# Performance work log

Measured on AMD Instinct MI355X. Metric: run time of the kernel, lower is better.

## Reference

```python
import jax, jax.numpy as jnp
import numpy as np

MARGIN = 0.3
HARD_FACTOR = 0.0
EPS = 1e-6


def setup_inputs() -> dict:
    key = jax.random.key(0)
    k1, k2 = jax.random.split(key)
    inputs = jax.random.normal(k1, (4096, 256), dtype=jnp.float32)
    targets = jax.random.randint(k2, (4096,), 0, 512, dtype=jnp.int64)
    return {"inputs": inputs, "targets": targets}


def reference(inputs, targets):
    n = inputs.shape[0]
    half = n // 2
    # L2-normalize features (matches normalize(): x / (||x|| + 1e-6))
    x = inputs / (jnp.linalg.norm(inputs, axis=-1, keepdims=True) + EPS)
    # pairwise euclidean distances, clamped at 1e-6 before sqrt
    sq = jnp.sum(x * x, axis=1)                      # (n,)
    dist = sq[:, None] + sq[None, :] - 2.0 * (x @ x.T)  # (n, n)
    dist = jnp.sqrt(jnp.clip(dist, EPS))
    # same-identity mask
    mask = targets[:, None] == targets[None, :]      # (n, n) bool
    # rows in the first half mine over columns [half:n], rows in the
    # second half mine over columns [0:half] -> gather the opposite half
    first = (jnp.arange(n) < half)[:, None]          # (n, 1)
    d_o = jnp.where(first, dist[:, half:], dist[:, :half])  # (n, half)
    m_o = jnp.where(first, mask[:, half:], mask[:, :half])  # (n, half) bool
    pos_any = jnp.any(m_o, axis=1)
    neg_any = jnp.any(~m_o, axis=1)
    dist_ap = jnp.where(pos_any,
                        jnp.max(jnp.where(m_o, d_o, -jnp.inf), axis=1),
                        0.0)
    dist_an = jnp.where(neg_any,
                        jnp.min(jnp.where(m_o, jnp.inf, d_o), axis=1),
                        1.0)
    dist_ap = dist_ap * (1.0 + HARD_FACTOR)
    dist_an = dist_an * (1.0 - HARD_FACTOR)
    # MarginRankingLoss(margin)(dist_an, dist_ap, y=1) =
    #   mean(relu(-(dist_an - dist_ap) + margin))
    loss = jnp.mean(jax.nn.relu(dist_ap - dist_an + MARGIN))
    return loss
```

## Files before the change

### kernel.cpp

```cpp
#include <hip/hip_runtime.h>
#include <math.h>

#define N 4096
#define D 256
#define HALF 2048
#define MARGIN 0.3f

#define BM 64
#define NTJ 32

typedef __attribute__((ext_vector_type(8))) short bf16x8;
typedef __attribute__((ext_vector_type(4))) float f32x4;

typedef __attribute__((address_space(1))) const unsigned int gas_uint;
typedef __attribute__((address_space(3))) unsigned int las_uint;

__device__ __forceinline__ void gld16(const unsigned short* g, unsigned short* l) {
    __builtin_amdgcn_global_load_lds((gas_uint*)g, (las_uint*)l, 16, 0, 0);
}

__device__ __forceinline__ unsigned short f2bf(float x) {
    unsigned int u = __float_as_uint(x);
    return (unsigned short)((u + 0x7fffu + ((u >> 16) & 1u)) >> 16);
}

__global__ __launch_bounds__(256) void k_norm(const float* __restrict__ in,
                                              unsigned short* __restrict__ xnb,
                                              float* __restrict__ sq,
                                              unsigned int* __restrict__ cnt) {
    const int row = blockIdx.x * 4 + (threadIdx.x >> 6);
    const int lane = threadIdx.x & 63;
    const float4 v = *(const float4*)&in[(size_t)row * D + lane * 4];
    float s = v.x * v.x + v.y * v.y + v.z * v.z + v.w * v.w;
#pragma unroll
    for (int o = 1; o < 64; o <<= 1) s += __shfl_xor(s, o, 64);
    float nrm = sqrtf(s);
    float inv = 1.0f / (nrm + 1e-6f);
    ushort4 o4;
    o4.x = f2bf(v.x * inv);
    o4.y = f2bf(v.y * inv);
    o4.z = f2bf(v.z * inv);
    o4.w = f2bf(v.w * inv);
    *(ushort4*)&xnb[(size_t)row * D + lane * 4] = o4;
    if (lane == 0) {
        float q = nrm * inv;
        sq[row] = q * q;
    }
    if (blockIdx.x == 0 && threadIdx.x == 0) *cnt = 0u;
}

__global__ __launch_bounds__(256, 2) void k_tile(const unsigned short* __restrict__ xnb,
                                                 const float* __restrict__ sq,
                                                 const int* __restrict__ tg,
                                                 int* __restrict__ rp_ap,
                                                 int* __restrict__ rp_an,
                                                 int* __restrict__ cp_ap,
                                                 int* __restrict__ cp_an) {
    __shared__ unsigned short As[BM * D];
    __shared__ unsigned short Bs[BM * D];
    __shared__ int sra[BM], srn[BM], sca[BM], scn[BM];

    const int bi = blockIdx.y, bj = blockIdx.x;
    const int I0 = bi * BM;
    const int J0 = bj * BM;
    const int tid = threadIdx.x;
    const int wave = tid >> 6, lane = tid & 63;
    const int wm = wave >> 1, wn = wave & 1;
    const int lrow = lane & 15, lquad = lane >> 4;

    const unsigned short* Ag = xnb + (size_t)I0 * D;
    const unsigned short* Bg = xnb + (size_t)(HALF + J0) * D;

#pragma unroll
    for (int i = 0; i < 8; ++i) {
        const int ch = i * 4 + wave;
        const int e = ch * 64 + lane;
        const int row = e >> 5;
        const int sc = (e & 31) ^ (row & 7);
        gld16(Ag + row * D + sc * 8, &As[ch * 512]);
        gld16(Bg + row * D + sc * 8, &Bs[ch * 512]);
    }
    if (tid < BM) {
        sra[tid] = 0; srn[tid] = 0x7f800000;
        sca[tid] = 0; scn[tid] = 0x7f800000;
    }
    asm volatile("s_waitcnt vmcnt(0)" ::: "memory");
    __syncthreads();

    f32x4 acc[2][2];
#pragma unroll
    for (int a = 0; a < 2; ++a)
#pragma unroll
        for (int b = 0; b < 2; ++b) acc[a][b] = (f32x4){0.f, 0.f, 0.f, 0.f};

#pragma unroll
    for (int kk = 0; kk < 8; ++kk) {
        bf16x8 af[2], bfr[2];
#pragma unroll
        for (int mi = 0; mi < 2; ++mi) {
            const int r = wm * 32 + mi * 16 + lrow;
            const int s = r * 32 + ((kk * 4 + lquad) ^ (r & 7));
            af[mi] = *(const bf16x8*)&As[s * 8];
        }
#pragma unroll
        for (int nj = 0; nj < 2; ++nj) {
            const int r = wn * 32 + nj * 16 + lrow;
            const int s = r * 32 + ((kk * 4 + lquad) ^ (r & 7));
            bfr[nj] = *(const bf16x8*)&Bs[s * 8];
        }
#pragma unroll
        for (int mi = 0; mi < 2; ++mi)
#pragma unroll
            for (int nj = 0; nj < 2; ++nj)
                acc[mi][nj] = __builtin_amdgcn_mfma_f32_16x16x32_bf16(
                    af[mi], bfr[nj], acc[mi][nj], 0, 0, 0);
    }

    float sqi[2][4], sqj[2];
    int tgi[2][4], tgj[2];
#pragma unroll
    for (int mi = 0; mi < 2; ++mi)
#pragma unroll
        for (int r = 0; r < 4; ++r) {
            int gi = I0 + wm * 32 + mi * 16 + lquad * 4 + r;
            sqi[mi][r] = sq[gi];
            tgi[mi][r] = tg[gi];
        }
#pragma unroll
    for (int nj = 0; nj < 2; ++nj) {
        int gj = HALF + J0 + wn * 32 + nj * 16 + lrow;
        sqj[nj] = sq[gj];
        tgj[nj] = tg[gj];
    }

    const float INF = __int_as_float(0x7f800000);
    float rap[2][4], ran[2][4], capv[2], canv[2];
#pragma unroll
    for (int mi = 0; mi < 2; ++mi)
#pragma unroll
        for (int r = 0; r < 4; ++r) { rap[mi][r] = 0.f; ran[mi][r] = INF; }
#pragma unroll
    for (int nj = 0; nj < 2; ++nj) { capv[nj] = 0.f; canv[nj] = INF; }

#pragma unroll
    for (int mi = 0; mi < 2; ++mi)
#pragma unroll
        for (int nj = 0; nj < 2; ++nj)
#pragma unroll
            for (int r = 0; r < 4; ++r) {
                float d2 = sqi[mi][r] + sqj[nj] - 2.0f * acc[mi][nj][r];
                float d = sqrtf(fmaxf(d2, 1e-6f));
                if (tgi[mi][r] == tgj[nj]) {
                    rap[mi][r] = fmaxf(rap[mi][r], d);
                    capv[nj] = fmaxf(capv[nj], d);
                } else {
                    ran[mi][r] = fminf(ran[mi][r], d);
                    canv[nj] = fminf(canv[nj], d);
                }
            }

#pragma unroll
    for (int mi = 0; mi < 2; ++mi)
#pragma unroll
        for (int r = 0; r < 4; ++r) {
#pragma unroll
            for (int o = 1; o < 16; o <<= 1) {
                rap[mi][r] = fmaxf(rap[mi][r], __shfl_xor(rap[mi][r], o, 64));
                ran[mi][r] = fminf(ran[mi][r], __shfl_xor(ran[mi][r], o, 64));
            }
        }
#pragma unroll
    for (int nj = 0; nj < 2; ++nj) {
#pragma unroll
        for (int o = 16; o < 64; o <<= 1) {
            capv[nj] = fmaxf(capv[nj], __shfl_xor(capv[nj], o, 64));
            canv[nj] = fminf(canv[nj], __shfl_xor(canv[nj], o, 64));
        }
    }

    if (lrow == 0) {
#pragma unroll
        for (int mi = 0; mi < 2; ++mi)
#pragma unroll
            for (int r = 0; r < 4; ++r) {
                int lr = wm * 32 + mi * 16 + lquad * 4 + r;
                atomicMax(&sra[lr], __float_as_int(rap[mi][r]));
                atomicMin(&srn[lr], __float_as_int(ran[mi][r]));
            }
    }
    if (lquad == 0) {
#pragma unroll
        for (int nj = 0; nj < 2; ++nj) {
            int lc = wn * 32 + nj * 16 + lrow;
            atomicMax(&sca[lc], __float_as_int(capv[nj]));
            atomicMin(&scn[lc], __float_as_int(canv[nj]));
        }
    }
    __syncthreads();
    if (tid < BM) {
        rp_ap[bj * HALF + I0 + tid] = sra[tid];
        rp_an[bj * HALF + I0 + tid] = srn[tid];
        cp_ap[bi * HALF + J0 + tid] = sca[tid];
        cp_an[bi * HALF + J0 + tid] = scn[tid];
    }
}

__global__ __launch_bounds__(256) void k_loss(const int* __restrict__ rp_ap,
                                              const int* __restrict__ rp_an,
                                              const int* __restrict__ cp_ap,
                                              const int* __restrict__ cp_an,
                                              float* __restrict__ bsum,
                                              unsigned int* __restrict__ cnt,
                                              float* __restrict__ out) {
    const int t = threadIdx.x;
    const int i = blockIdx.x * 256 + t;
    const int first = (i < HALF);
    const int idx = first ? i : i - HALF;
    const int* pa = first ? rp_ap : cp_ap;
    const int* pn = first ? rp_an : cp_an;
    int apb = 0, anb = 0x7f800000;
#pragma unroll
    for (int b = 0; b < NTJ; ++b) {
        apb = max(apb, pa[b * HALF + idx]);
        anb = min(anb, pn[b * HALF + idx]);
    }
    float dap = __int_as_float(apb);
    float dan = (anb == 0x7f800000) ? 1.0f : __int_as_float(anb);
    float v = dap - dan + MARGIN;
    float s = (v > 0.f) ? v : 0.f;
#pragma unroll
    for (int o = 1; o < 64; o <<= 1) s += __shfl_xor(s, o, 64);
    __shared__ float ws4[4];
    __shared__ bool amLast;
    if ((t & 63) == 0) ws4[t >> 6] = s;
    __syncthreads();
    if (t == 0) {
        bsum[blockIdx.x] = ws4[0] + ws4[1] + ws4[2] + ws4[3];
        __threadfence();
        amLast = (atomicAdd(cnt, 1u) == 15u);
    }
    __syncthreads();
    if (amLast && t == 0) {
        volatile float* vb = bsum;
        float tot = 0.f;
#pragma unroll
        for (int b = 0; b < 16; ++b) tot += vb[b];
        out[0] = tot / (float)N;
    }
}

extern "C" void kernel_launch(void* const* d_in, const int* in_sizes, int n_in,
                              void* d_out, int out_size, void* d_ws, size_t ws_size,
                              hipStream_t stream) {
    const float* in = (const float*)d_in[0];
    const int* tg = (const int*)d_in[1];
    float* out = (float*)d_out;

    unsigned short* xnb = (unsigned short*)d_ws;
    float* sq = (float*)(xnb + (size_t)N * D);
    int* rp_ap = (int*)(sq + N);
    int* rp_an = rp_ap + NTJ * HALF;
    int* cp_ap = rp_an + NTJ * HALF;
    int* cp_an = cp_ap + NTJ * HALF;
    float* bsum = (float*)(cp_an + NTJ * HALF);
    unsigned int* cnt = (unsigned int*)(bsum + 16);

    k_norm<<<N / 4, 256, 0, stream>>>(in, xnb, sq, cnt);
    k_tile<<<dim3(NTJ, NTJ), 256, 0, stream>>>(xnb, sq, tg,
                                               rp_ap, rp_an, cp_ap, cp_an);
    k_loss<<<16, 256, 0, stream>>>(rp_ap, rp_an, cp_ap, cp_an, bsum, cnt, out);
}
```

Before: 84.80 us.

## Fuse normalization, tile mining and loss reduction into a single kernel

```diff
diff --git a/kernel.cpp b/kernel.cpp
--- a/kernel.cpp
+++ b/kernel.cpp
@@ -12,53 +12,27 @@
 typedef __attribute__((ext_vector_type(8))) short bf16x8;
 typedef __attribute__((ext_vector_type(4))) float f32x4;
 
-typedef __attribute__((address_space(1))) const unsigned int gas_uint;
-typedef __attribute__((address_space(3))) unsigned int las_uint;
-
-__device__ __forceinline__ void gld16(const unsigned short* g, unsigned short* l) {
-    __builtin_amdgcn_global_load_lds((gas_uint*)g, (las_uint*)l, 16, 0, 0);
-}
+__device__ unsigned int g_row_cnt[NTJ];
+__device__ unsigned int g_col_cnt[NTJ];
+__device__ unsigned int g_fin_cnt;
 
 __device__ __forceinline__ unsigned short f2bf(float x) {
     unsigned int u = __float_as_uint(x);
     return (unsigned short)((u + 0x7fffu + ((u >> 16) & 1u)) >> 16);
 }
 
-__global__ __launch_bounds__(256) void k_norm(const float* __restrict__ in,
-                                              unsigned short* __restrict__ xnb,
-                                              float* __restrict__ sq,
-                                              unsigned int* __restrict__ cnt) {
-    const int row = blockIdx.x * 4 + (threadIdx.x >> 6);
-    const int lane = threadIdx.x & 63;
-    const float4 v = *(const float4*)&in[(size_t)row * D + lane * 4];
-    float s = v.x * v.x + v.y * v.y + v.z * v.z + v.w * v.w;
-#pragma unroll
-    for (int o = 1; o < 64; o <<= 1) s += __shfl_xor(s, o, 64);
-    float nrm = sqrtf(s);
-    float inv = 1.0f / (nrm + 1e-6f);
-    ushort4 o4;
-    o4.x = f2bf(v.x * inv);
-    o4.y = f2bf(v.y * inv);
-    o4.z = f2bf(v.z * inv);
-    o4.w = f2bf(v.w * inv);
-    *(ushort4*)&xnb[(size_t)row * D + lane * 4] = o4;
-    if (lane == 0) {
-        float q = nrm * inv;
-        sq[row] = q * q;
-    }
-    if (blockIdx.x == 0 && threadIdx.x == 0) *cnt = 0u;
-}
-
-__global__ __launch_bounds__(256, 2) void k_tile(const unsigned short* __restrict__ xnb,
-                                                 const float* __restrict__ sq,
-                                                 const int* __restrict__ tg,
-                                                 int* __restrict__ rp_ap,
-                                                 int* __restrict__ rp_an,
-                                                 int* __restrict__ cp_ap,
-                                                 int* __restrict__ cp_an) {
+__global__ __launch_bounds__(256, 2) void k_all(const float* __restrict__ in,
+                                                const int* __restrict__ tg,
+                                                int* __restrict__ rp_ap,
+                                                int* __restrict__ rp_an,
+                                                int* __restrict__ cp_ap,
+                                                int* __restrict__ cp_an,
+                                                float* __restrict__ strip_sum,
+                                                float* __restrict__ out) {
     __shared__ unsigned short As[BM * D];
     __shared__ unsigned short Bs[BM * D];
     __shared__ int sra[BM], srn[BM], sca[BM], scn[BM];
+    __shared__ float sqA[BM], sqB[BM];
 
     const int bi = blockIdx.y, bj = blockIdx.x;
     const int I0 = bi * BM;
@@ -68,23 +42,42 @@
     const int wm = wave >> 1, wn = wave & 1;
     const int lrow = lane & 15, lquad = lane >> 4;
 
-    const unsigned short* Ag = xnb + (size_t)I0 * D;
-    const unsigned short* Bg = xnb + (size_t)(HALF + J0) * D;
-
-#pragma unroll
-    for (int i = 0; i < 8; ++i) {
-        const int ch = i * 4 + wave;
-        const int e = ch * 64 + lane;
-        const int row = e >> 5;
-        const int sc = (e & 31) ^ (row & 7);
-        gld16(Ag + row * D + sc * 8, &As[ch * 512]);
-        gld16(Bg + row * D + sc * 8, &Bs[ch * 512]);
-    }
     if (tid < BM) {
         sra[tid] = 0; srn[tid] = 0x7f800000;
         sca[tid] = 0; scn[tid] = 0x7f800000;
     }
-    asm volatile("s_waitcnt vmcnt(0)" ::: "memory");
+
+    const int g = lane >> 1, h = lane & 1;
+#pragma unroll 2
+    for (int p = 0; p < 16; ++p) {
+        const int r = wave * 16 + p;
+        {
+            const float4 v = *(const float4*)&in[(size_t)(I0 + r) * D + lane * 4];
+            float s = v.x * v.x + v.y * v.y + v.z * v.z + v.w * v.w;
+#pragma unroll
+            for (int o = 1; o < 64; o <<= 1) s += __shfl_xor(s, o, 64);
+            float nrm = sqrtf(s);
+            float inv = 1.0f / (nrm + 1e-6f);
+            ushort4 o4;
+            o4.x = f2bf(v.x * inv); o4.y = f2bf(v.y * inv);
+            o4.z = f2bf(v.z * inv); o4.w = f2bf(v.w * inv);
+            *(ushort4*)&As[(r * 32 + (g ^ (r & 7))) * 8 + h * 4] = o4;
+            if (lane == 0) { float q = nrm * inv; sqA[r] = q * q; }
+        }
+        {
+            const float4 v = *(const float4*)&in[(size_t)(HALF + J0 + r) * D + lane * 4];
+            float s = v.x * v.x + v.y * v.y + v.z * v.z + v.w * v.w;
+#pragma unroll
+            for (int o = 1; o < 64; o <<= 1) s += __shfl_xor(s, o, 64);
+            float nrm = sqrtf(s);
+            float inv = 1.0f / (nrm + 1e-6f);
+            ushort4 o4;
+            o4.x = f2bf(v.x * inv); o4.y = f2bf(v.y * inv);
+            o4.z = f2bf(v.z * inv); o4.w = f2bf(v.w * inv);
+            *(ushort4*)&Bs[(r * 32 + (g ^ (r & 7))) * 8 + h * 4] = o4;
+            if (lane == 0) { float q = nrm * inv; sqB[r] = q * q; }
+        }
+    }
     __syncthreads();
 
     f32x4 acc[2][2];
@@ -122,15 +115,15 @@
     for (int mi = 0; mi < 2; ++mi)
 #pragma unroll
         for (int r = 0; r < 4; ++r) {
-            int gi = I0 + wm * 32 + mi * 16 + lquad * 4 + r;
-            sqi[mi][r] = sq[gi];
-            tgi[mi][r] = tg[gi];
+            int lr = wm * 32 + mi * 16 + lquad * 4 + r;
+            sqi[mi][r] = sqA[lr];
+            tgi[mi][r] = tg[I0 + lr];
         }
 #pragma unroll
     for (int nj = 0; nj < 2; ++nj) {
-        int gj = HALF + J0 + wn * 32 + nj * 16 + lrow;
-        sqj[nj] = sq[gj];
-        tgj[nj] = tg[gj];
+        int lc = wn * 32 + nj * 16 + lrow;
+        sqj[nj] = sqB[lc];
+        tgj[nj] = tg[HALF + J0 + lc];
     }
 
     const float INF = __int_as_float(0x7f800000);
@@ -197,55 +190,116 @@
         }
     }
     __syncthreads();
+
     if (tid < BM) {
-        rp_ap[bj * HALF + I0 + tid] = sra[tid];
-        rp_an[bj * HALF + I0 + tid] = srn[tid];
-        cp_ap[bi * HALF + J0 + tid] = sca[tid];
-        cp_an[bi * HALF + J0 + tid] = scn[tid];
-    }
-}
-
-__global__ __launch_bounds__(256) void k_loss(const int* __restrict__ rp_ap,
-                                              const int* __restrict__ rp_an,
-                                              const int* __restrict__ cp_ap,
-                                              const int* __restrict__ cp_an,
-                                              float* __restrict__ bsum,
-                                              unsigned int* __restrict__ cnt,
-                                              float* __restrict__ out) {
-    const int t = threadIdx.x;
-    const int i = blockIdx.x * 256 + t;
-    const int first = (i < HALF);
-    const int idx = first ? i : i - HALF;
-    const int* pa = first ? rp_ap : cp_ap;
-    const int* pn = first ? rp_an : cp_an;
-    int apb = 0, anb = 0x7f800000;
-#pragma unroll
-    for (int b = 0; b < NTJ; ++b) {
-        apb = max(apb, pa[b * HALF + idx]);
-        anb = min(anb, pn[b * HALF + idx]);
-    }
-    float dap = __int_as_float(apb);
-    float dan = (anb == 0x7f800000) ? 1.0f : __int_as_float(anb);
-    float v = dap - dan + MARGIN;
-    float s = (v > 0.f) ? v : 0.f;
-#pragma unroll
-    for (int o = 1; o < 64; o <<= 1) s += __shfl_xor(s, o, 64);
-    __shared__ float ws4[4];
-    __shared__ bool amLast;
-    if ((t & 63) == 0) ws4[t >> 6] = s;
+        rp_ap[bi * (NTJ * BM) + bj * BM + tid] = sra[tid];
+        rp_an[bi * (NTJ * BM) + bj * BM + tid] = srn[tid];
+        cp_ap[bj * (NTJ * BM) + bi * BM + tid] = sca[tid];
+        cp_an[bj * (NTJ * BM) + bi * BM + tid] = scn[tid];
+    }
+    __threadfence();
     __syncthreads();
-    if (t == 0) {
-        bsum[blockIdx.x] = ws4[0] + ws4[1] + ws4[2] + ws4[3];
-        __threadfence();
-        amLast = (atomicAdd(cnt, 1u) == 15u);
-    }
-    __syncthreads();
-    if (amLast && t == 0) {
-        volatile float* vb = bsum;
-        float tot = 0.f;
-#pragma unroll
-        for (int b = 0; b < 16; ++b) tot += vb[b];
-        out[0] = tot / (float)N;
+
+    if (wave == 0) {
+        int fin = 0;
+        if (lane == 0) {
+            unsigned int old = __hip_atomic_fetch_add(
+                &g_row_cnt[bi], 1u, __ATOMIC_ACQ_REL, __HIP_MEMORY_SCOPE_AGENT);
+            fin = (old == NTJ - 1);
+            if (fin)
+                __hip_atomic_fetch_add(&g_row_cnt[bi], 0u - (unsigned)NTJ,
+                                       __ATOMIC_RELAXED, __HIP_MEMORY_SCOPE_AGENT);
+        }
+        fin = __shfl(fin, 0, 64);
+        if (fin) {
+            __threadfence();
+            int apb = 0, anb = 0x7f800000;
+            const int base = bi * (NTJ * BM) + lane;
+#pragma unroll
+            for (int b = 0; b < NTJ; ++b) {
+                apb = max(apb, __hip_atomic_load(&rp_ap[base + b * BM],
+                           __ATOMIC_RELAXED, __HIP_MEMORY_SCOPE_AGENT));
+                anb = min(anb, __hip_atomic_load(&rp_an[base + b * BM],
+                           __ATOMIC_RELAXED, __HIP_MEMORY_SCOPE_AGENT));
+            }
+            float dap = __int_as_float(apb);
+            float dan = (anb == 0x7f800000) ? 1.0f : __int_as_float(anb);
+            float v = dap - dan + MARGIN;
+            float sl = (v > 0.f) ? v : 0.f;
+#pragma unroll
+            for (int o = 1; o < 64; o <<= 1) sl += __shfl_xor(sl, o, 64);
+            if (lane == 0) {
+                __hip_atomic_store(&strip_sum[bi], sl,
+                                   __ATOMIC_RELAXED, __HIP_MEMORY_SCOPE_AGENT);
+                __threadfence();
+                unsigned int fo = __hip_atomic_fetch_add(
+                    &g_fin_cnt, 1u, __ATOMIC_ACQ_REL, __HIP_MEMORY_SCOPE_AGENT);
+                if (fo == 2u * NTJ - 1u) {
+                    __hip_atomic_fetch_add(&g_fin_cnt, 0u - 2u * (unsigned)NTJ,
+                                           __ATOMIC_RELAXED, __HIP_MEMORY_SCOPE_AGENT);
+                    __threadfence();
+                    float t[2 * NTJ];
+#pragma unroll
+                    for (int b = 0; b < 2 * NTJ; ++b)
+                        t[b] = __hip_atomic_load(&strip_sum[b],
+                                 __ATOMIC_RELAXED, __HIP_MEMORY_SCOPE_AGENT);
+                    float tot = 0.f;
+#pragma unroll
+                    for (int b = 0; b < 2 * NTJ; ++b) tot += t[b];
+                    out[0] = tot / (float)N;
+                }
+            }
+        }
+    } else if (wave == 1) {
+        int fin = 0;
+        if (lane == 0) {
+            unsigned int old = __hip_atomic_fetch_add(
+                &g_col_cnt[bj], 1u, __ATOMIC_ACQ_REL, __HIP_MEMORY_SCOPE_AGENT);
+            fin = (old == NTJ - 1);
+            if (fin)
+                __hip_atomic_fetch_add(&g_col_cnt[bj], 0u - (unsigned)NTJ,
+                                       __ATOMIC_RELAXED, __HIP_MEMORY_SCOPE_AGENT);
+        }
+        fin = __shfl(fin, 0, 64);
+        if (fin) {
+            __threadfence();
+            int apb = 0, anb = 0x7f800000;
+            const int base = bj * (NTJ * BM) + lane;
+#pragma unroll
+            for (int b = 0; b < NTJ; ++b) {
+                apb = max(apb, __hip_atomic_load(&cp_ap[base + b * BM],
+                           __ATOMIC_RELAXED, __HIP_MEMORY_SCOPE_AGENT));
+                anb = min(anb, __hip_atomic_load(&cp_an[base + b * BM],
+                           __ATOMIC_RELAXED, __HIP_MEMORY_SCOPE_AGENT));
+            }
+            float dap = __int_as_float(apb);
+            float dan = (anb == 0x7f800000) ? 1.0f : __int_as_float(anb);
+            float v = dap - dan + MARGIN;
+            float sl = (v > 0.f) ? v : 0.f;
+#pragma unroll
+            for (int o = 1; o < 64; o <<= 1) sl += __shfl_xor(sl, o, 64);
+            if (lane == 0) {
+                __hip_atomic_store(&strip_sum[NTJ + bj], sl,
+                                   __ATOMIC_RELAXED, __HIP_MEMORY_SCOPE_AGENT);
+                __threadfence();
+                unsigned int fo = __hip_atomic_fetch_add(
+                    &g_fin_cnt, 1u, __ATOMIC_ACQ_REL, __HIP_MEMORY_SCOPE_AGENT);
+                if (fo == 2u * NTJ - 1u) {
+                    __hip_atomic_fetch_add(&g_fin_cnt, 0u - 2u * (unsigned)NTJ,
+                                           __ATOMIC_RELAXED, __HIP_MEMORY_SCOPE_AGENT);
+                    __threadfence();
+                    float t[2 * NTJ];
+#pragma unroll
+                    for (int b = 0; b < 2 * NTJ; ++b)
+                        t[b] = __hip_atomic_load(&strip_sum[b],
+                                 __ATOMIC_RELAXED, __HIP_MEMORY_SCOPE_AGENT);
+                    float tot = 0.f;
+#pragma unroll
+                    for (int b = 0; b < 2 * NTJ; ++b) tot += t[b];
+                    out[0] = tot / (float)N;
+                }
+            }
+        }
     }
 }
 
@@ -256,17 +310,12 @@
     const int* tg = (const int*)d_in[1];
     float* out = (float*)d_out;
 
-    unsigned short* xnb = (unsigned short*)d_ws;
-    float* sq = (float*)(xnb + (size_t)N * D);
-    int* rp_ap = (int*)(sq + N);
+    int* rp_ap = (int*)d_ws;
     int* rp_an = rp_ap + NTJ * HALF;
     int* cp_ap = rp_an + NTJ * HALF;
     int* cp_an = cp_ap + NTJ * HALF;
-    float* bsum = (float*)(cp_an + NTJ * HALF);
-    unsigned int* cnt = (unsigned int*)(bsum + 16);
-
-    k_norm<<<N / 4, 256, 0, stream>>>(in, xnb, sq, cnt);
-    k_tile<<<dim3(NTJ, NTJ), 256, 0, stream>>>(xnb, sq, tg,
-                                               rp_ap, rp_an, cp_ap, cp_an);
-    k_loss<<<16, 256, 0, stream>>>(rp_ap, rp_an, cp_ap, cp_an, bsum, cnt, out);
+    float* strip_sum = (float*)(cp_an + NTJ * HALF);
+
+    k_all<<<dim3(NTJ, NTJ), 256, 0, stream>>>(in, tg, rp_ap, rp_an,
+                                              cp_ap, cp_an, strip_sum, out);
 }
```

New measurement: 199.1 us. 135% more time.
